# Performance work log

Measured on AMD Instinct MI355X. Metric: run time of the kernel, lower is better.

The kernel has to match this reference:

```python
import jax, jax.numpy as jnp
import numpy as np

B, S = 64, 2048
ENC_DIM, DEC_DIM, ATT_DIM = 1024, 1024, 512


def setup_inputs() -> dict:
    key = jax.random.key(0)
    k1, k2, k3, k4, k5, k6 = jax.random.split(key, 6)
    # parameters follow torch kaiming_uniform_(a=sqrt(5)) -> U(-1/sqrt(fan_in), 1/sqrt(fan_in)) scale approx
    def uni(k, shape, fan_in):
        b = 1.0 / np.sqrt(fan_in)
        return jax.random.uniform(k, shape, jnp.float32, -b, b)
    return {
        "decoder_hidden": jax.random.normal(k1, (B, DEC_DIM), jnp.float32),
        "encoder_outputs": jax.random.normal(k2, (B, S, ENC_DIM), jnp.float32),
        "mask": jax.random.randint(k3, (B, S), 0, 2) > 0,
        "W_enc": uni(k4, (ATT_DIM, ENC_DIM), ENC_DIM),   # encoder_projection.weight
        "W_dec": uni(k5, (ATT_DIM, DEC_DIM), DEC_DIM),   # decoder_projection.weight
        "W_energy": uni(k6, (1, ATT_DIM), ATT_DIM),      # energy_projection.weight
    }


def reference(decoder_hidden, encoder_outputs, mask, W_enc, W_dec, W_energy):
    # decoder_features: [B, 1, A]
    dec_feat = (decoder_hidden @ W_dec.T)[:, None, :]
    # encoder_features: [B, S, A]
    enc_feat = jnp.einsum("bse,ae->bsa", encoder_outputs, W_enc)
    energy = jnp.tanh(enc_feat + dec_feat)                     # [B, S, A]
    scores = jnp.einsum("bsa,a->bs", energy, W_energy[0])      # [B, S]
    scores = jnp.where(mask, jnp.finfo(scores.dtype).min, scores)
    attention_weights = jax.nn.softmax(scores, axis=-1)        # [B, S]
    context = jnp.einsum("bs,bse->be", attention_weights, encoder_outputs)
    return context, attention_weights
```

## Files before the change

kernel.cpp:

```cpp
#include <hip/hip_runtime.h>
#include <stdint.h>

#define B_ 64
#define S_ 2048
#define E_ 1024
#define D_ 1024
#define A_ 512
#define M_ (B_*S_)

typedef __attribute__((ext_vector_type(8))) short short8;
typedef __attribute__((ext_vector_type(4))) float floatx4;

typedef __attribute__((address_space(3))) void       lds_void_t;
typedef const __attribute__((address_space(1))) void gbl_void_t;

__device__ __forceinline__ unsigned short f2bf(float f) {
    union { float f; uint32_t u; } v; v.f = f;
    uint32_t u = v.u;
    return (unsigned short)((u + 0x7FFF + ((u >> 16) & 1)) >> 16);
}

__global__ void k_convert_wenc(const float* __restrict__ wenc,
                               unsigned short* __restrict__ wencS) {
    int slot = blockIdx.x * 256 + threadIdx.x;
    int kt = slot >> 11;
    int kq = (slot >> 9) & 3;
    int n  = slot & 511;
    const float4* src = (const float4*)(wenc + (size_t)n * E_ + kt * 32 + kq * 8);
    float4 a = src[0], b = src[1];
    short8 o;
    o[0] = (short)f2bf(a.x); o[1] = (short)f2bf(a.y);
    o[2] = (short)f2bf(a.z); o[3] = (short)f2bf(a.w);
    o[4] = (short)f2bf(b.x); o[5] = (short)f2bf(b.y);
    o[6] = (short)f2bf(b.z); o[7] = (short)f2bf(b.w);
    *(short8*)(wencS + (size_t)slot * 8) = o;
}

__global__ void k_dec_feat(const float* __restrict__ dh,
                           const float* __restrict__ wdec,
                           float* __restrict__ df) {
    __shared__ float h[1056];
    int b  = blockIdx.x >> 3;
    int a0 = (blockIdx.x & 7) * 64;
    int t  = threadIdx.x;
    {
        float4 v = ((const float4*)(dh + (size_t)b * D_))[t];
        int e0 = t * 4;
        *(float4*)(h + (e0 >> 8) * 264 + (e0 & 255)) = v;
    }
    __syncthreads();
    int a  = a0 + (t >> 2);
    int kq = t & 3;
    const float4* wr = (const float4*)(wdec + (size_t)a * D_ + kq * 256);
    const float4* hh = (const float4*)(h + kq * 264);
    float acc = 0.f;
    #pragma unroll 8
    for (int k4 = 0; k4 < 64; ++k4) {
        float4 w = wr[k4];
        float4 x = hh[k4];
        acc += w.x*x.x + w.y*x.y + w.z*x.z + w.w*x.w;
    }
    acc += __shfl_xor(acc, 1);
    acc += __shfl_xor(acc, 2);
    if ((t & 3) == 0) df[b * A_ + a] = acc;
}

#define BM 64
#define BK 32
#define AROW 40

__global__ __launch_bounds__(256, 2) void k_scores(
    const float* __restrict__ enc,
    const unsigned short* __restrict__ wencS,
    const float* __restrict__ df,
    const float* __restrict__ wE,
    float* __restrict__ scores)
{
    __shared__ unsigned short As[BM * AROW];
    __shared__ unsigned short Bs[4 * 512 * 8];
    __shared__ float ps[4][BM];

    const int tid  = threadIdx.x;
    const int wave = tid >> 6;
    const int lane = tid & 63;
    const int m0   = blockIdx.x * BM;
    const int b    = m0 >> 11;

    floatx4 acc[4][8];
    #pragma unroll
    for (int i = 0; i < 4; ++i)
        #pragma unroll
        for (int j = 0; j < 8; ++j) acc[i][j] = (floatx4)0.f;

    const int m_a = tid >> 2;
    const int j_a = tid & 3;
    const float* aptr = enc + (size_t)(m0 + m_a) * E_ + j_a * 8;

    const int n0w   = wave * 128;
    const int row16 = lane >> 4;
    const int col   = lane & 15;

    for (int kt = 0; kt < E_ / BK; ++kt) {
        if (kt) __syncthreads();
        float4 a0 = *(const float4*)(aptr + kt * BK);
        float4 a1 = *(const float4*)(aptr + kt * BK + 4);
        #pragma unroll
        for (int r = 0; r < 8; ++r) {
            int s = r * 256 + tid;
            const unsigned short* g = wencS + ((size_t)kt * 2048 + s) * 8;
            unsigned short* l = &Bs[(size_t)(r * 256 + wave * 64) * 8];
            __builtin_amdgcn_global_load_lds((gbl_void_t*)g, (lds_void_t*)l, 16, 0, 0);
        }
        short8 apk;
        apk[0] = (short)f2bf(a0.x); apk[1] = (short)f2bf(a0.y);
        apk[2] = (short)f2bf(a0.z); apk[3] = (short)f2bf(a0.w);
        apk[4] = (short)f2bf(a1.x); apk[5] = (short)f2bf(a1.y);
        apk[6] = (short)f2bf(a1.z); apk[7] = (short)f2bf(a1.w);
        *(short8*)(&As[m_a * AROW + j_a * 8]) = apk;
        __syncthreads();
        short8 af[4];
        #pragma unroll
        for (int mt = 0; mt < 4; ++mt)
            af[mt] = *(const short8*)(&As[(mt * 16 + col) * AROW + row16 * 8]);
        short8 bfr[8];
        #pragma unroll
        for (int nt = 0; nt < 8; ++nt)
            bfr[nt] = *(const short8*)(&Bs[(size_t)(row16 * 512 + n0w + nt * 16 + col) * 8]);
        #pragma unroll
        for (int mt = 0; mt < 4; ++mt)
            #pragma unroll
            for (int nt = 0; nt < 8; ++nt)
                acc[mt][nt] = __builtin_amdgcn_mfma_f32_16x16x32_bf16(
                    af[mt], bfr[nt], acc[mt][nt], 0, 0, 0);
    }

    float part[4][4];
    #pragma unroll
    for (int mt = 0; mt < 4; ++mt)
        #pragma unroll
        for (int r = 0; r < 4; ++r) part[mt][r] = 0.f;

    #pragma unroll
    for (int nt = 0; nt < 8; ++nt) {
        int n   = n0w + nt * 16 + col;
        float d = df[b * A_ + n];
        float w = wE[n];
        #pragma unroll
        for (int mt = 0; mt < 4; ++mt)
            #pragma unroll
            for (int r = 0; r < 4; ++r) {
                float x  = acc[mt][nt][r] + d;
                float ex = __expf(2.f * x);
                float th = 1.f - 2.f / (ex + 1.f);
                part[mt][r] += w * th;
            }
    }
    #pragma unroll
    for (int mt = 0; mt < 4; ++mt)
        #pragma unroll
        for (int r = 0; r < 4; ++r) {
            float v = part[mt][r];
            v += __shfl_xor(v, 1);
            v += __shfl_xor(v, 2);
            v += __shfl_xor(v, 4);
            v += __shfl_xor(v, 8);
            part[mt][r] = v;
        }
    if (col == 0) {
        #pragma unroll
        for (int mt = 0; mt < 4; ++mt)
            #pragma unroll
            for (int r = 0; r < 4; ++r)
                ps[wave][mt * 16 + row16 * 4 + r] = part[mt][r];
    }
    __syncthreads();
    if (tid < BM)
        scores[m0 + tid] = ps[0][tid] + ps[1][tid] + ps[2][tid] + ps[3][tid];
}

__global__ void k_softmax(const float* __restrict__ scores,
                          const int* __restrict__ mask,
                          float* __restrict__ weights) {
    __shared__ float red[8];
    int b = blockIdx.x, t = threadIdx.x;
    float v[8];
    #pragma unroll
    for (int i = 0; i < 8; ++i) {
        int s = t + i * 256;
        float x = scores[b * S_ + s];
        v[i] = mask[b * S_ + s] ? -3.402823466e38f : x;
    }
    float mx = v[0];
    #pragma unroll
    for (int i = 1; i < 8; ++i) mx = fmaxf(mx, v[i]);
    #pragma unroll
    for (int o = 32; o; o >>= 1) mx = fmaxf(mx, __shfl_xor(mx, o));
    if ((t & 63) == 0) red[t >> 6] = mx;
    __syncthreads();
    mx = fmaxf(fmaxf(red[0], red[1]), fmaxf(red[2], red[3]));

    float e[8], sum = 0.f;
    #pragma unroll
    for (int i = 0; i < 8; ++i) { e[i] = __expf(v[i] - mx); sum += e[i]; }
    #pragma unroll
    for (int o = 32; o; o >>= 1) sum += __shfl_xor(sum, o);
    if ((t & 63) == 0) red[4 + (t >> 6)] = sum;
    __syncthreads();
    sum = red[4] + red[5] + red[6] + red[7];
    float inv = 1.f / sum;
    #pragma unroll
    for (int i = 0; i < 8; ++i)
        weights[b * S_ + t + i * 256] = e[i] * inv;
}

__global__ void k_context(const float* __restrict__ enc,
                          const float* __restrict__ weights,
                          float* __restrict__ ctx) {
    int b  = blockIdx.x >> 3;
    int sc = blockIdx.x & 7;
    int t  = threadIdx.x;
    const float4* ep = (const float4*)(enc + (size_t)b * S_ * E_ + (size_t)sc * 256 * E_) + t;
    const float*  wp = weights + b * S_ + sc * 256;
    float4 acc = {0.f, 0.f, 0.f, 0.f};
    for (int s0 = 0; s0 < 256; s0 += 8) {
        float4 x[8];
        #pragma unroll
        for (int i = 0; i < 8; ++i)
            x[i] = ep[(size_t)(s0 + i) * (E_ / 4)];
        #pragma unroll
        for (int i = 0; i < 8; ++i) {
            float w = wp[s0 + i];
            acc.x += w * x[i].x; acc.y += w * x[i].y;
            acc.z += w * x[i].z; acc.w += w * x[i].w;
        }
    }
    float* o = ctx + (size_t)b * E_ + t * 4;
    atomicAdd(o + 0, acc.x); atomicAdd(o + 1, acc.y);
    atomicAdd(o + 2, acc.z); atomicAdd(o + 3, acc.w);
}

extern "C" void kernel_launch(void* const* d_in, const int* in_sizes, int n_in,
                              void* d_out, int out_size, void* d_ws, size_t ws_size,
                              hipStream_t stream) {
    const float* dh   = (const float*)d_in[0];
    const float* enc  = (const float*)d_in[1];
    const int*   mask = (const int*)  d_in[2];
    const float* wenc = (const float*)d_in[3];
    const float* wdec = (const float*)d_in[4];
    const float* wE   = (const float*)d_in[5];

    float* out     = (float*)d_out;
    float* ctx     = out;
    float* weights = out + B_ * E_;

    unsigned short* wencS = (unsigned short*)d_ws;
    float* df     = (float*)((char*)d_ws + (size_t)A_ * E_ * 2);
    float* scores = df + B_ * A_;

    hipMemsetAsync(ctx, 0, (size_t)B_ * E_ * sizeof(float), stream);
    k_convert_wenc<<<256, 256, 0, stream>>>(wenc, wencS);
    k_dec_feat<<<B_ * 8, 256, 0, stream>>>(dh, wdec, df);
    k_scores<<<M_ / BM, 256, 0, stream>>>(enc, wencS, df, wE, scores);
    k_softmax<<<B_, 256, 0, stream>>>(scores, mask, weights);
    k_context<<<B_ * 8, 256, 0, stream>>>(enc, weights, ctx);
}
```

Before: 901.3 us.

## Compact unmasked positions and skip masked rows in scores and context

Adds a per-batch compaction kernel that builds an index list of unmasked sequence positions and a count. The scores GEMM, softmax and context reduction then work only on those rows, gathering encoder rows by index and exiting early on blocks past the count. Masked positions get weight zero through a zeroed output buffer, and an all-masked row falls back to uniform weights. Roughly half of the GEMM and context work is skipped for the random mask, at the cost of an extra kernel and gathered memory access.

```diff
diff --git a/kernel.cpp b/kernel.cpp
--- a/kernel.cpp
+++ b/kernel.cpp
@@ -65,6 +65,46 @@
     if ((t & 3) == 0) df[b * A_ + a] = acc;
 }
 
+__global__ void k_compact(const int* __restrict__ mask,
+                          int* __restrict__ idx,
+                          int* __restrict__ cnt) {
+    __shared__ int wsum[4];
+    __shared__ int s_total;
+    int b = blockIdx.x, t = threadIdx.x;
+    int lane = t & 63, wv = t >> 6;
+    const int* mrow = mask + b * S_;
+    int base = t * 8;
+    unsigned keep = 0;
+    int c = 0;
+    #pragma unroll
+    for (int i = 0; i < 8; ++i) {
+        if (!mrow[base + i]) { keep |= 1u << i; ++c; }
+    }
+    int v = c;
+    #pragma unroll
+    for (int o = 1; o < 64; o <<= 1) {
+        int u = __shfl_up(v, o);
+        if (lane >= o) v += u;
+    }
+    if (lane == 63) wsum[wv] = v;
+    __syncthreads();
+    int wbase = 0;
+    for (int w = 0; w < wv; ++w) wbase += wsum[w];
+    int o = wbase + v - c;
+    int* orow = idx + b * S_;
+    #pragma unroll
+    for (int i = 0; i < 8; ++i)
+        if (keep & (1u << i)) orow[o++] = base + i;
+    if (t == 255) { int tot = wbase + v; s_total = tot; cnt[b] = tot; }
+    __syncthreads();
+    int total = s_total;
+    if (total == 0) {
+        for (int j = t; j < S_; j += 256) orow[j] = j;
+    } else {
+        for (int j = total + t; j < S_; j += 256) orow[j] = 0;
+    }
+}
+
 #define BM 64
 #define BK 32
 #define AROW 40
@@ -74,8 +114,15 @@
     const unsigned short* __restrict__ wencS,
     const float* __restrict__ df,
     const float* __restrict__ wE,
+    const int* __restrict__ idx,
+    const int* __restrict__ cnt,
     float* __restrict__ scores)
 {
+    const int bid = blockIdx.x;
+    const int b   = bid >> 5;
+    const int c   = bid & 31;
+    if (c * BM >= cnt[b]) return;
+
     __shared__ unsigned short As[BM * AROW];
     __shared__ unsigned short Bs[4 * 512 * 8];
     __shared__ float ps[4][BM];
@@ -83,8 +130,6 @@
     const int tid  = threadIdx.x;
     const int wave = tid >> 6;
     const int lane = tid & 63;
-    const int m0   = blockIdx.x * BM;
-    const int b    = m0 >> 11;
 
     floatx4 acc[4][8];
     #pragma unroll
@@ -94,7 +139,8 @@
 
     const int m_a = tid >> 2;
     const int j_a = tid & 3;
-    const float* aptr = enc + (size_t)(m0 + m_a) * E_ + j_a * 8;
+    const int row = idx[b * S_ + c * BM + m_a];
+    const float* aptr = enc + ((size_t)b * S_ + row) * E_ + j_a * 8;
 
     const int n0w   = wave * 128;
     const int row16 = lane >> 4;
@@ -175,24 +221,37 @@
     }
     __syncthreads();
     if (tid < BM)
-        scores[m0 + tid] = ps[0][tid] + ps[1][tid] + ps[2][tid] + ps[3][tid];
+        scores[b * S_ + c * BM + tid] = ps[0][tid] + ps[1][tid] + ps[2][tid] + ps[3][tid];
 }
 
 __global__ void k_softmax(const float* __restrict__ scores,
-                          const int* __restrict__ mask,
-                          float* __restrict__ weights) {
+                          const int* __restrict__ idx,
+                          const int* __restrict__ cnt,
+                          float* __restrict__ weights,
+                          float* __restrict__ wc,
+                          int* __restrict__ ecnt) {
     __shared__ float red[8];
     int b = blockIdx.x, t = threadIdx.x;
+    int n = cnt[b];
+    if (n == 0) {
+        float u = 1.f / (float)S_;
+        for (int j = t; j < S_; j += 256) {
+            weights[b * S_ + j] = u;
+            wc[b * S_ + j] = u;
+        }
+        if (t == 0) ecnt[b] = S_;
+        return;
+    }
+    if (t == 0) ecnt[b] = n;
+    const float* srow = scores + b * S_;
     float v[8];
+    float mx = -3.402823466e38f;
     #pragma unroll
     for (int i = 0; i < 8; ++i) {
-        int s = t + i * 256;
-        float x = scores[b * S_ + s];
-        v[i] = mask[b * S_ + s] ? -3.402823466e38f : x;
-    }
-    float mx = v[0];
-    #pragma unroll
-    for (int i = 1; i < 8; ++i) mx = fmaxf(mx, v[i]);
+        int j = t + i * 256;
+        v[i] = (j < n) ? srow[j] : -3.402823466e38f;
+        mx = fmaxf(mx, v[i]);
+    }
     #pragma unroll
     for (int o = 32; o; o >>= 1) mx = fmaxf(mx, __shfl_xor(mx, o));
     if ((t & 63) == 0) red[t >> 6] = mx;
@@ -208,30 +267,45 @@
     __syncthreads();
     sum = red[4] + red[5] + red[6] + red[7];
     float inv = 1.f / sum;
-    #pragma unroll
-    for (int i = 0; i < 8; ++i)
-        weights[b * S_ + t + i * 256] = e[i] * inv;
+    int nceil = (n + 127) & ~127;
+    #pragma unroll
+    for (int i = 0; i < 8; ++i) {
+        int j = t + i * 256;
+        if (j < n) {
+            float w = e[i] * inv;
+            weights[b * S_ + idx[b * S_ + j]] = w;
+            wc[b * S_ + j] = w;
+        } else if (j < nceil) {
+            wc[b * S_ + j] = 0.f;
+        }
+    }
 }
 
 __global__ void k_context(const float* __restrict__ enc,
-                          const float* __restrict__ weights,
+                          const float* __restrict__ wc,
+                          const int* __restrict__ idx,
+                          const int* __restrict__ ecnt,
                           float* __restrict__ ctx) {
-    int b  = blockIdx.x >> 3;
-    int sc = blockIdx.x & 7;
+    int b  = blockIdx.x >> 4;
+    int sc = blockIdx.x & 15;
+    if (sc * 128 >= ecnt[b]) return;
     int t  = threadIdx.x;
-    const float4* ep = (const float4*)(enc + (size_t)b * S_ * E_ + (size_t)sc * 256 * E_) + t;
-    const float*  wp = weights + b * S_ + sc * 256;
+    const int*   ip = idx + b * S_ + sc * 128;
+    const float* wp = wc  + b * S_ + sc * 128;
+    const float4* ebase = (const float4*)(enc + (size_t)b * S_ * E_);
     float4 acc = {0.f, 0.f, 0.f, 0.f};
-    for (int s0 = 0; s0 < 256; s0 += 8) {
-        float4 x[8];
-        #pragma unroll
-        for (int i = 0; i < 8; ++i)
-            x[i] = ep[(size_t)(s0 + i) * (E_ / 4)];
+    for (int s0 = 0; s0 < 128; s0 += 8) {
+        float4 x[8]; float w[8];
         #pragma unroll
         for (int i = 0; i < 8; ++i) {
-            float w = wp[s0 + i];
-            acc.x += w * x[i].x; acc.y += w * x[i].y;
-            acc.z += w * x[i].z; acc.w += w * x[i].w;
+            int r = ip[s0 + i];
+            w[i] = wp[s0 + i];
+            x[i] = ebase[(size_t)r * (E_ / 4) + t];
+        }
+        #pragma unroll
+        for (int i = 0; i < 8; ++i) {
+            acc.x += w[i] * x[i].x; acc.y += w[i] * x[i].y;
+            acc.z += w[i] * x[i].z; acc.w += w[i] * x[i].w;
         }
     }
     float* o = ctx + (size_t)b * E_ + t * 4;
@@ -256,11 +330,16 @@
     unsigned short* wencS = (unsigned short*)d_ws;
     float* df     = (float*)((char*)d_ws + (size_t)A_ * E_ * 2);
     float* scores = df + B_ * A_;
-
-    hipMemsetAsync(ctx, 0, (size_t)B_ * E_ * sizeof(float), stream);
+    int*   idx    = (int*)(scores + (size_t)B_ * S_);
+    int*   cnt    = idx + (size_t)B_ * S_;
+    int*   ecnt   = cnt + B_;
+    float* wc     = (float*)(ecnt + B_);
+
+    hipMemsetAsync(out, 0, (size_t)(B_ * E_ + B_ * S_) * sizeof(float), stream);
     k_convert_wenc<<<256, 256, 0, stream>>>(wenc, wencS);
     k_dec_feat<<<B_ * 8, 256, 0, stream>>>(dh, wdec, df);
-    k_scores<<<M_ / BM, 256, 0, stream>>>(enc, wencS, df, wE, scores);
-    k_softmax<<<B_, 256, 0, stream>>>(scores, mask, weights);
-    k_context<<<B_ * 8, 256, 0, stream>>>(enc, weights, ctx);
-}
+    k_compact<<<B_, 256, 0, stream>>>(mask, idx, cnt);
+    k_scores<<<M_ / BM, 256, 0, stream>>>(enc, wencS, df, wE, idx, cnt, scores);
+    k_softmax<<<B_, 256, 0, stream>>>(scores, idx, cnt, weights, wc, ecnt);
+    k_context<<<B_ * 16, 256, 0, stream>>>(enc, wc, idx, ecnt, ctx);
+}
```

After: 863.8 us. -4.2%, faster.
